# Kernel optimization log

Hardware: AMD Instinct MI355X
Metric: run time of the kernel (lower is better)

The kernel has to match this reference:

```python
import jax, jax.numpy as jnp
import numpy as np

EPS = 1e-8


def setup_inputs() -> dict:
    key = jax.random.key(0)
    ks = jax.random.split(key, 8)
    B, N, D = 8, 1024, 256
    x = jax.random.normal(ks[0], (B, N, D), dtype=jnp.float32)
    y = jax.random.normal(ks[1], (B, N, D), dtype=jnp.float32)
    coords = jax.random.normal(ks[2], (N, N, 6), dtype=jnp.float32)
    # xavier-ish init for U, kaiming-ish for S1/S2
    U = jax.random.normal(ks[3], (D, D), dtype=jnp.float32) * (1.0 / np.sqrt(D))
    S1 = jax.random.normal(ks[4], (D, 1), dtype=jnp.float32)
    S2 = jax.random.normal(ks[5], (D, 1), dtype=jnp.float32)
    gating = jnp.asarray(1.0, dtype=jnp.float32)
    h_temp = jnp.asarray(0.1, dtype=jnp.float32)
    p_temp = jnp.asarray(1.0, dtype=jnp.float32)
    # trunc_normal_(a=0, b=1): std-normal truncated to [0, 1]
    pos_emb = jax.random.truncated_normal(ks[6], 0.0, 1.0, (N, 6, 1)).astype(jnp.float32)
    return {"x": x, "y": y, "coords": coords, "U": U, "S1": S1, "S2": S2,
            "gating": gating, "h_temp": h_temp, "p_temp": p_temp, "pos_emb": pos_emb}


def _spectral(x, U, S):
    # x @ U.T @ diag(|S|) @ U  ==  ((x @ U.T) * |S|) @ U
    s = jnp.abs(S[:, 0])
    return ((x @ U.T) * s) @ U


def reference(x, y, coords, U, S1, S2, gating, h_temp, p_temp, pos_emb):
    B, N, D = x.shape
    scale = D ** (-0.5)
    xs = jnp.stack([_spectral(x, U, S1), _spectral(x, U, S2)], axis=1)  # [B,2,N,D]
    # patch attention scores: [B,2,N,N]
    patch_score = jax.nn.softmax(jnp.einsum('bknd,bmd->bknm', xs, y) * scale, axis=-1)
    # positional scores, shared across batch and the 2 spectral branches: [N,N]
    pos_logits = -jnp.abs(p_temp) * jnp.einsum('nmc,ncq->nm', coords, pos_emb)
    pos_score = jax.nn.softmax(pos_logits, axis=-1)
    g = jax.nn.sigmoid(gating)
    attn = (1.0 - g) * patch_score + g * pos_score[None, None]  # [B,2,N,N]
    # entropy over key axis -> [B,N,2]
    entropy = jnp.sum(-attn * jnp.log(attn + EPS), axis=-1).transpose(0, 2, 1)
    hmap = 2.0 - 2.0 * jax.nn.sigmoid(h_temp * entropy)  # [B,N,2]
    fgbg = hmap[..., 0] >= hmap[..., 1]
    route = jax.lax.stop_gradient(
        jnp.stack([fgbg, ~fgbg], axis=-1).astype(hmap.dtype))  # [B,N,2]
    heat_map = jnp.sum(hmap * route, axis=-1, keepdims=True)  # [B,N,1]
    attn_sel = jnp.sum(attn * route.transpose(0, 2, 1)[..., None], axis=1)  # [B,N,N]
    out = attn_sel @ y  # [B,N,D]
    return (out, heat_map)
```

## Files before the change

### kernel.cpp

```cpp
#include <hip/hip_runtime.h>
#include <hip/hip_bf16.h>


#define NB 8
#define NN_ 1024
#define ND 256

typedef __bf16 bf16x8 __attribute__((ext_vector_type(8)));
typedef __bf16 bf16x4 __attribute__((ext_vector_type(4)));
typedef float f32x4 __attribute__((ext_vector_type(4)));

__device__ inline float wred_sum(float v) {
#pragma unroll
    for (int o = 32; o; o >>= 1) v += __shfl_xor(v, o, 64);
    return v;
}
__device__ inline float wred_max(float v) {
#pragma unroll
    for (int o = 32; o; o >>= 1) v = fmaxf(v, __shfl_xor(v, o, 64));
    return v;
}
__device__ inline float bred_sum(float v, float* red) {
    v = wred_sum(v);
    int w = threadIdx.x >> 6;
    __syncthreads();
    if ((threadIdx.x & 63) == 0) red[w] = v;
    __syncthreads();
    return red[0] + red[1] + red[2] + red[3];
}
__device__ inline float bred_max(float v, float* red) {
    v = wred_max(v);
    int w = threadIdx.x >> 6;
    __syncthreads();
    if ((threadIdx.x & 63) == 0) red[w] = v;
    __syncthreads();
    return fmaxf(fmaxf(red[0], red[1]), fmaxf(red[2], red[3]));
}

__global__ __launch_bounds__(256) void pos_kernel(
    const float* __restrict__ coords, const float* __restrict__ pos_emb,
    const float* __restrict__ p_temp, float* __restrict__ posS) {
    __shared__ float red[4];
    const int n = blockIdx.x;
    const int tid = threadIdx.x;
    const float pt = -fabsf(p_temp[0]);
    float pe[6];
#pragma unroll
    for (int c = 0; c < 6; ++c) pe[c] = pos_emb[n * 6 + c];
    const float* cr = coords + (long)n * NN_ * 6;
    float l[4];
#pragma unroll
    for (int j = 0; j < 4; ++j) {
        const int m = tid * 4 + j;
        const float* cp = cr + m * 6;
        float d = 0.f;
#pragma unroll
        for (int c = 0; c < 6; ++c) d += cp[c] * pe[c];
        l[j] = pt * d;
    }
    float mx = fmaxf(fmaxf(l[0], l[1]), fmaxf(l[2], l[3]));
    mx = bred_max(mx, red);
    float e[4], s = 0.f;
#pragma unroll
    for (int j = 0; j < 4; ++j) { e[j] = expf(l[j] - mx); s += e[j]; }
    s = bred_sum(s, red);
    const float inv = 1.f / s;
    float4 o;
    o.x = e[0] * inv; o.y = e[1] * inv; o.z = e[2] * inv; o.w = e[3] * inv;
    *(float4*)(posS + (long)n * NN_ + tid * 4) = o;
}

__global__ __launch_bounds__(256) void conv_split(
    const float* __restrict__ src, __bf16* __restrict__ hi,
    __bf16* __restrict__ lo, int n4) {
    int i = blockIdx.x * 256 + threadIdx.x;
    const int stride = gridDim.x * 256;
    for (; i < n4; i += stride) {
        float4 v = ((const float4*)src)[i];
        bf16x4 h, l;
        h[0] = (__bf16)v.x; l[0] = (__bf16)(v.x - (float)h[0]);
        h[1] = (__bf16)v.y; l[1] = (__bf16)(v.y - (float)h[1]);
        h[2] = (__bf16)v.z; l[2] = (__bf16)(v.z - (float)h[2]);
        h[3] = (__bf16)v.w; l[3] = (__bf16)(v.w - (float)h[3]);
        ((bf16x4*)hi)[i] = h;
        ((bf16x4*)lo)[i] = l;
    }
}

__global__ __launch_bounds__(256) void conv_U(
    const float* __restrict__ U, const float* __restrict__ S1,
    const float* __restrict__ S2, __bf16* __restrict__ Uh, __bf16* __restrict__ Ul,
    __bf16* __restrict__ Wh, __bf16* __restrict__ Wl) {
    const int n = blockIdx.x, k = threadIdx.x;
    float u = U[n * ND + k];
    __bf16 h = (__bf16)u;
    Uh[n * ND + k] = h; Ul[n * ND + k] = (__bf16)(u - (float)h);
    float ukn = U[k * ND + n];
    float w1 = ukn * fabsf(S1[k]);
    float w2 = ukn * fabsf(S2[k]);
    __bf16 h1 = (__bf16)w1, h2 = (__bf16)w2;
    Wh[n * ND + k] = h1;             Wl[n * ND + k] = (__bf16)(w1 - (float)h1);
    Wh[65536 + n * ND + k] = h2;     Wl[65536 + n * ND + k] = (__bf16)(w2 - (float)h2);
}

__global__ __launch_bounds__(256) void prep_y(
    const float* __restrict__ y, __bf16* __restrict__ yt,
    __bf16* __restrict__ Yh, __bf16* __restrict__ Yl) {
    __shared__ __bf16 t[64][72];
    const int b = blockIdx.z;
    const int m0 = blockIdx.x * 64, d0 = blockIdx.y * 64;
    const int tid = threadIdx.x;
    const int c = tid & 15;
    const int r = tid >> 4;
#pragma unroll
    for (int p = 0; p < 4; ++p) {
        const int row = r + p * 16;
        const long gi = ((long)b * NN_ + m0 + row) * ND + d0 + c * 4;
        float4 v = *(const float4*)(y + gi);
        bf16x4 h, l;
        h[0] = (__bf16)v.x; l[0] = (__bf16)(v.x - (float)h[0]);
        h[1] = (__bf16)v.y; l[1] = (__bf16)(v.y - (float)h[1]);
        h[2] = (__bf16)v.z; l[2] = (__bf16)(v.z - (float)h[2]);
        h[3] = (__bf16)v.w; l[3] = (__bf16)(v.w - (float)h[3]);
        *(bf16x4*)(Yh + gi) = h;
        *(bf16x4*)(Yl + gi) = l;
        t[c * 4 + 0][row] = h[0]; t[c * 4 + 1][row] = h[1];
        t[c * 4 + 2][row] = h[2]; t[c * 4 + 3][row] = h[3];
    }
    __syncthreads();
#pragma unroll
    for (int p = 0; p < 4; ++p) {
        const int d = r + p * 16;
        bf16x4 o;
        o[0] = t[d][c * 4 + 0]; o[1] = t[d][c * 4 + 1];
        o[2] = t[d][c * 4 + 2]; o[3] = t[d][c * 4 + 3];
        *(bf16x4*)(yt + ((long)b * ND + d0 + d) * NN_ + m0 + c * 4) = o;
    }
}

template <int BN, bool SPLIT, int OUTM>
__global__ __launch_bounds__(256) void mgemm(
    const __bf16* __restrict__ Ah, const __bf16* __restrict__ Al,
    const __bf16* __restrict__ Bh, const __bf16* __restrict__ Bl,
    float* __restrict__ C, __bf16* __restrict__ Ch, __bf16* __restrict__ Cl,
    int M, int N, int K,
    long sA1, long sA2, int divA, long sB1, int divB, long sC, float alpha) {
    constexpr int BM = 128, BK = 32, RS = 40;
    constexpr int NBUF = SPLIT ? 2 : 1;
    constexpr int NF = BN / 32;
    __shared__ __bf16 As[NBUF][BM * RS];
    __shared__ __bf16 Bs[NBUF][BN * RS];

    const int z = blockIdx.z;
    const long aoff = (long)(z / divA) * sA1 + (long)(z % divA) * sA2;
    const long boff = (long)(z / divB) * sB1;
    Ah += aoff; if (SPLIT) Al += aoff;
    Bh += boff; if (SPLIT) Bl += boff;

    const int tid = threadIdx.x;
    const int bm = blockIdx.y * BM, bn = blockIdx.x * BN;
    const int wave = tid >> 6, lane = tid & 63;
    const int wm = wave >> 1, wn = wave & 1;
    const int quad = lane >> 4, l16 = lane & 15;

    f32x4 acc[4][NF];
#pragma unroll
    for (int i = 0; i < 4; ++i)
#pragma unroll
        for (int j = 0; j < NF; ++j) acc[i][j] = (f32x4){0.f, 0.f, 0.f, 0.f};

    const int arow = tid >> 1, ak = (tid & 1) * 16;

    for (int k0 = 0; k0 < K; k0 += BK) {
        {
            const long g = (long)(bm + arow) * K + k0 + ak;
            *(bf16x8*)&As[0][arow * RS + ak] = *(const bf16x8*)(Ah + g);
            *(bf16x8*)&As[0][arow * RS + ak + 8] = *(const bf16x8*)(Ah + g + 8);
            if (SPLIT) {
                *(bf16x8*)&As[1][arow * RS + ak] = *(const bf16x8*)(Al + g);
                *(bf16x8*)&As[1][arow * RS + ak + 8] = *(const bf16x8*)(Al + g + 8);
            }
        }
        if (BN == 128) {
            const long g = (long)(bn + arow) * K + k0 + ak;
            *(bf16x8*)&Bs[0][arow * RS + ak] = *(const bf16x8*)(Bh + g);
            *(bf16x8*)&Bs[0][arow * RS + ak + 8] = *(const bf16x8*)(Bh + g + 8);
            if (SPLIT) {
                *(bf16x8*)&Bs[1][arow * RS + ak] = *(const bf16x8*)(Bl + g);
                *(bf16x8*)&Bs[1][arow * RS + ak + 8] = *(const bf16x8*)(Bl + g + 8);
            }
        } else {
            const int brow = tid >> 2, bk = (tid & 3) * 8;
            const long g = (long)(bn + brow) * K + k0 + bk;
            *(bf16x8*)&Bs[0][brow * RS + bk] = *(const bf16x8*)(Bh + g);
            if (SPLIT)
                *(bf16x8*)&Bs[1][brow * RS + bk] = *(const bf16x8*)(Bl + g);
        }
        __syncthreads();

        bf16x8 a_h[4], a_l[4], b_h[NF], b_l[NF];
#pragma unroll
        for (int mi = 0; mi < 4; ++mi) {
            const int r = (wm * 64 + mi * 16 + l16) * RS + quad * 8;
            a_h[mi] = *(const bf16x8*)&As[0][r];
            if (SPLIT) a_l[mi] = *(const bf16x8*)&As[1][r];
        }
#pragma unroll
        for (int ni = 0; ni < NF; ++ni) {
            const int r = (wn * (BN / 2) + ni * 16 + l16) * RS + quad * 8;
            b_h[ni] = *(const bf16x8*)&Bs[0][r];
            if (SPLIT) b_l[ni] = *(const bf16x8*)&Bs[1][r];
        }
#pragma unroll
        for (int mi = 0; mi < 4; ++mi)
#pragma unroll
            for (int ni = 0; ni < NF; ++ni) {
                acc[mi][ni] = __builtin_amdgcn_mfma_f32_16x16x32_bf16(
                    a_h[mi], b_h[ni], acc[mi][ni], 0, 0, 0);
                if (SPLIT) {
                    acc[mi][ni] = __builtin_amdgcn_mfma_f32_16x16x32_bf16(
                        a_h[mi], b_l[ni], acc[mi][ni], 0, 0, 0);
                    acc[mi][ni] = __builtin_amdgcn_mfma_f32_16x16x32_bf16(
                        a_l[mi], b_h[ni], acc[mi][ni], 0, 0, 0);
                }
            }
        __syncthreads();
    }

    C += (long)z * sC; Ch += (long)z * sC; Cl += (long)z * sC;
#pragma unroll
    for (int mi = 0; mi < 4; ++mi) {
        const int row0 = bm + wm * 64 + mi * 16 + quad * 4;
#pragma unroll
        for (int ni = 0; ni < NF; ++ni) {
            const int col = bn + wn * (BN / 2) + ni * 16 + l16;
#pragma unroll
            for (int r = 0; r < 4; ++r) {
                const float v = acc[mi][ni][r] * alpha;
                const long idx = (long)(row0 + r) * N + col;
                if (OUTM == 0) {
                    C[idx] = v;
                } else {
                    const __bf16 h = (__bf16)v;
                    Ch[idx] = h;
                    Cl[idx] = (__bf16)(v - (float)h);
                }
            }
        }
    }
}

__global__ __launch_bounds__(256) void blend_kernel(
    const float* __restrict__ S, const float* __restrict__ pos,
    const float* __restrict__ gating, const float* __restrict__ h_temp,
    float* __restrict__ heat, __bf16* __restrict__ Pb) {
    __shared__ float red[4];
    const int bn = blockIdx.x;
    const int b = bn >> 10, n = bn & 1023;
    const float* S0 = S + ((long)(b * 2 + 0) * NN_ + n) * NN_;
    const float* S1 = S + ((long)(b * 2 + 1) * NN_ + n) * NN_;
    const int tid = threadIdx.x;

    float4 l0 = *(const float4*)(S0 + tid * 4);
    float4 l1 = *(const float4*)(S1 + tid * 4);
    float4 pv = *(const float4*)(pos + (long)n * NN_ + tid * 4);

    float m0 = fmaxf(fmaxf(l0.x, l0.y), fmaxf(l0.z, l0.w));
    m0 = bred_max(m0, red);
    float e0x = expf(l0.x - m0), e0y = expf(l0.y - m0),
          e0z = expf(l0.z - m0), e0w = expf(l0.w - m0);
    float s0 = bred_sum(e0x + e0y + e0z + e0w, red);
    const float i0 = 1.f / s0;
    float m1 = fmaxf(fmaxf(l1.x, l1.y), fmaxf(l1.z, l1.w));
    m1 = bred_max(m1, red);
    float e1x = expf(l1.x - m1), e1y = expf(l1.y - m1),
          e1z = expf(l1.z - m1), e1w = expf(l1.w - m1);
    float s1 = bred_sum(e1x + e1y + e1z + e1w, red);
    const float i1 = 1.f / s1;

    const float g = 1.f / (1.f + expf(-gating[0]));
    const float cg = 1.f - g;

    float a0[4], a1[4];
    a0[0] = cg * (e0x * i0) + g * pv.x; a0[1] = cg * (e0y * i0) + g * pv.y;
    a0[2] = cg * (e0z * i0) + g * pv.z; a0[3] = cg * (e0w * i0) + g * pv.w;
    a1[0] = cg * (e1x * i1) + g * pv.x; a1[1] = cg * (e1y * i1) + g * pv.y;
    a1[2] = cg * (e1z * i1) + g * pv.z; a1[3] = cg * (e1w * i1) + g * pv.w;

    float ent0 = 0.f, ent1 = 0.f;
#pragma unroll
    for (int j = 0; j < 4; ++j) {
        ent0 -= a0[j] * logf(a0[j] + 1e-8f);
        ent1 -= a1[j] * logf(a1[j] + 1e-8f);
    }
    ent0 = bred_sum(ent0, red);
    ent1 = bred_sum(ent1, red);

    const float ht = h_temp[0];
    const float hm0 = 2.f - 2.f / (1.f + expf(-ht * ent0));
    const float hm1 = 2.f - 2.f / (1.f + expf(-ht * ent1));
    const bool fg = (hm0 >= hm1);
    if (tid == 0) heat[bn] = fg ? hm0 : hm1;

    bf16x4 o;
    o[0] = (__bf16)(fg ? a0[0] : a1[0]);
    o[1] = (__bf16)(fg ? a0[1] : a1[1]);
    o[2] = (__bf16)(fg ? a0[2] : a1[2]);
    o[3] = (__bf16)(fg ? a0[3] : a1[3]);
    *(bf16x4*)(Pb + ((long)b * NN_ + n) * NN_ + tid * 4) = o;
}

extern "C" void kernel_launch(void* const* d_in, const int* in_sizes, int n_in,
                              void* d_out, int out_size, void* d_ws, size_t ws_size,
                              hipStream_t stream) {
    const float* x      = (const float*)d_in[0];
    const float* y      = (const float*)d_in[1];
    const float* coords = (const float*)d_in[2];
    const float* U      = (const float*)d_in[3];
    const float* S1p    = (const float*)d_in[4];
    const float* S2p    = (const float*)d_in[5];
    const float* gating = (const float*)d_in[6];
    const float* h_temp = (const float*)d_in[7];
    const float* p_temp = (const float*)d_in[8];
    const float* pos_emb= (const float*)d_in[9];

    float* out  = (float*)d_out;
    float* heat = out + (long)NB * NN_ * ND;

    char* ws = (char*)d_ws;
    const long MB = 1 << 20;
    float*  Sf  = (float*)(ws);
    float*  pos = (float*)(ws + 64 * MB);
    __bf16* Xh  = (__bf16*)(ws + 68 * MB);
    __bf16* Xl  = (__bf16*)(ws + 72 * MB);
    __bf16* XSh = (__bf16*)(ws + 68 * MB);
    __bf16* XSl = (__bf16*)(ws + 76 * MB);
    __bf16* Pb  = (__bf16*)(ws + 68 * MB);
    __bf16* yt  = (__bf16*)(ws + 84 * MB);
    __bf16* Yh  = (__bf16*)(ws + 88 * MB);
    __bf16* Yl  = (__bf16*)(ws + 92 * MB);
    __bf16* Th  = (__bf16*)(ws + 96 * MB);
    __bf16* Tl  = (__bf16*)(ws + 100 * MB);
    __bf16* Uh  = (__bf16*)(ws + 104 * MB);
    __bf16* Ul  = Uh + 65536;
    __bf16* Wh  = Uh + 2 * 65536;
    __bf16* Wl  = Uh + 4 * 65536;

    const long ND2 = (long)NN_ * ND;
    const long BND = (long)NB * ND2;

    pos_kernel<<<dim3(NN_), 256, 0, stream>>>(coords, pos_emb, p_temp, pos);
    conv_split<<<dim3(2048), 256, 0, stream>>>(x, Xh, Xl, (int)(BND / 4));
    prep_y<<<dim3(16, 4, NB), 256, 0, stream>>>(y, yt, Yh, Yl);
    conv_U<<<dim3(ND), ND, 0, stream>>>(U, S1p, S2p, Uh, Ul, Wh, Wl);

    mgemm<64, true, 1><<<dim3(4, 64, 1), 256, 0, stream>>>(
        Xh, Xl, Uh, Ul, nullptr, Th, Tl, NB * NN_, ND, ND,
        0, 0, 1, 0, 1, 0, 1.0f);

    mgemm<64, true, 1><<<dim3(4, 64, 2), 256, 0, stream>>>(
        Th, Tl, Wh, Wl, nullptr, XSh, XSl, NB * NN_, ND, ND,
        0, 0, 1, 65536, 1, BND, 1.0f);

    mgemm<128, true, 0><<<dim3(8, 8, NB * 2), 256, 0, stream>>>(
        XSh, XSl, Yh, Yl, Sf, nullptr, nullptr, NN_, NN_, ND,
        ND2, BND, 2, ND2, 2, (long)NN_ * NN_, 0.0625f);

    blend_kernel<<<dim3(NB * NN_), 256, 0, stream>>>(Sf, pos, gating, h_temp, heat, Pb);

    mgemm<64, false, 0><<<dim3(4, 8, NB), 256, 0, stream>>>(
        Pb, nullptr, yt, nullptr, out, nullptr, nullptr, NN_, ND, NN_,
        (long)NN_ * NN_, 0, 1, ND2, 1, ND2, 1.0f);

    (void)in_sizes; (void)n_in; (void)out_size; (void)ws_size;
}
```

Before: 224.2 us.

## Fold spectral projections into precomputed matrices and load GEMM tiles via global_load_lds

Precomputes M_s = U^T diag(|S|) U once per call in a small kernel, so x@M replaces two chained GEMMs and the intermediate T buffers are dropped. The GEMM kernel now loads tiles straight into LDS with global_load_lds using an XOR-swizzled, unpadded layout, and moves the barrier to the top of the loop. The positional kernel switches to coalesced strided rows with float2 loads. The M build is a naive serial loop of 256 iterations per thread and adds some rounding from the different factorisation.

```diff
diff --git a/kernel.cpp b/kernel.cpp
--- a/kernel.cpp
+++ b/kernel.cpp
@@ -1,5 +1,6 @@
 #include <hip/hip_runtime.h>
 #include <hip/hip_bf16.h>
+#include <stdint.h>
 
 
 #define NB 8
@@ -9,6 +10,12 @@
 typedef __bf16 bf16x8 __attribute__((ext_vector_type(8)));
 typedef __bf16 bf16x4 __attribute__((ext_vector_type(4)));
 typedef float f32x4 __attribute__((ext_vector_type(4)));
+
+__device__ inline void gl_lds(const __bf16* g, __bf16* l) {
+    auto gp = (const __attribute__((address_space(1))) uint32_t*)(uintptr_t)g;
+    auto lp = (__attribute__((address_space(3))) uint32_t*)(uintptr_t)l;
+    __builtin_amdgcn_global_load_lds(gp, lp, 16, 0, 0);
+}
 
 __device__ inline float wred_sum(float v) {
 #pragma unroll
@@ -51,12 +58,11 @@
     float l[4];
 #pragma unroll
     for (int j = 0; j < 4; ++j) {
-        const int m = tid * 4 + j;
-        const float* cp = cr + m * 6;
-        float d = 0.f;
-#pragma unroll
-        for (int c = 0; c < 6; ++c) d += cp[c] * pe[c];
-        l[j] = pt * d;
+        const int m = j * 256 + tid;
+        const float2* cp = (const float2*)(cr + (long)m * 6);
+        float2 c0 = cp[0], c1 = cp[1], c2 = cp[2];
+        l[j] = pt * (c0.x * pe[0] + c0.y * pe[1] + c1.x * pe[2] +
+                     c1.y * pe[3] + c2.x * pe[4] + c2.y * pe[5]);
     }
     float mx = fmaxf(fmaxf(l[0], l[1]), fmaxf(l[2], l[3]));
     mx = bred_max(mx, red);
@@ -65,9 +71,8 @@
     for (int j = 0; j < 4; ++j) { e[j] = expf(l[j] - mx); s += e[j]; }
     s = bred_sum(s, red);
     const float inv = 1.f / s;
-    float4 o;
-    o.x = e[0] * inv; o.y = e[1] * inv; o.z = e[2] * inv; o.w = e[3] * inv;
-    *(float4*)(posS + (long)n * NN_ + tid * 4) = o;
+#pragma unroll
+    for (int j = 0; j < 4; ++j) posS[(long)n * NN_ + j * 256 + tid] = e[j] * inv;
 }
 
 __global__ __launch_bounds__(256) void conv_split(
@@ -87,20 +92,21 @@
     }
 }
 
-__global__ __launch_bounds__(256) void conv_U(
+__global__ __launch_bounds__(256) void build_M(
     const float* __restrict__ U, const float* __restrict__ S1,
-    const float* __restrict__ S2, __bf16* __restrict__ Uh, __bf16* __restrict__ Ul,
-    __bf16* __restrict__ Wh, __bf16* __restrict__ Wl) {
-    const int n = blockIdx.x, k = threadIdx.x;
-    float u = U[n * ND + k];
-    __bf16 h = (__bf16)u;
-    Uh[n * ND + k] = h; Ul[n * ND + k] = (__bf16)(u - (float)h);
-    float ukn = U[k * ND + n];
-    float w1 = ukn * fabsf(S1[k]);
-    float w2 = ukn * fabsf(S2[k]);
-    __bf16 h1 = (__bf16)w1, h2 = (__bf16)w2;
-    Wh[n * ND + k] = h1;             Wl[n * ND + k] = (__bf16)(w1 - (float)h1);
-    Wh[65536 + n * ND + k] = h2;     Wl[65536 + n * ND + k] = (__bf16)(w2 - (float)h2);
+    const float* __restrict__ S2, __bf16* __restrict__ Mh,
+    __bf16* __restrict__ Ml) {
+    const int n = blockIdx.x, j = threadIdx.x;
+    float a1 = 0.f, a2 = 0.f;
+    for (int c = 0; c < ND; ++c) {
+        const float un = U[c * ND + n];
+        const float uj = U[c * ND + j];
+        a1 = fmaf(fabsf(S1[c]) * un, uj, a1);
+        a2 = fmaf(fabsf(S2[c]) * un, uj, a2);
+    }
+    const __bf16 h1 = (__bf16)a1, h2 = (__bf16)a2;
+    Mh[n * ND + j] = h1;            Ml[n * ND + j] = (__bf16)(a1 - (float)h1);
+    Mh[65536 + n * ND + j] = h2;    Ml[65536 + n * ND + j] = (__bf16)(a2 - (float)h2);
 }
 
 __global__ __launch_bounds__(256) void prep_y(
@@ -145,11 +151,11 @@
     float* __restrict__ C, __bf16* __restrict__ Ch, __bf16* __restrict__ Cl,
     int M, int N, int K,
     long sA1, long sA2, int divA, long sB1, int divB, long sC, float alpha) {
-    constexpr int BM = 128, BK = 32, RS = 40;
+    constexpr int BM = 128, BK = 32;
     constexpr int NBUF = SPLIT ? 2 : 1;
     constexpr int NF = BN / 32;
-    __shared__ __bf16 As[NBUF][BM * RS];
-    __shared__ __bf16 Bs[NBUF][BN * RS];
+    __shared__ __bf16 As[NBUF * BM * BK];
+    __shared__ __bf16 Bs[NBUF * BN * BK];
 
     const int z = blockIdx.z;
     const long aoff = (long)(z / divA) * sA1 + (long)(z % divA) * sA2;
@@ -169,47 +175,54 @@
 #pragma unroll
         for (int j = 0; j < NF; ++j) acc[i][j] = (f32x4){0.f, 0.f, 0.f, 0.f};
 
-    const int arow = tid >> 1, ak = (tid & 1) * 16;
+    const int srow = lane >> 2;
+    const int slot = lane & 3;
 
     for (int k0 = 0; k0 < K; k0 += BK) {
-        {
-            const long g = (long)(bm + arow) * K + k0 + ak;
-            *(bf16x8*)&As[0][arow * RS + ak] = *(const bf16x8*)(Ah + g);
-            *(bf16x8*)&As[0][arow * RS + ak + 8] = *(const bf16x8*)(Ah + g + 8);
-            if (SPLIT) {
-                *(bf16x8*)&As[1][arow * RS + ak] = *(const bf16x8*)(Al + g);
-                *(bf16x8*)&As[1][arow * RS + ak + 8] = *(const bf16x8*)(Al + g + 8);
-            }
+        __syncthreads();
+#pragma unroll
+        for (int i = 0; i < 2; ++i) {
+            const int r0 = wave * 32 + i * 16;
+            const int row = r0 + srow;
+            const int chunk = slot ^ ((row >> 1) & 3);
+            const long g = (long)(bm + row) * K + k0 + chunk * 8;
+            gl_lds(Ah + g, &As[r0 * 32]);
+            if (SPLIT) gl_lds(Al + g, &As[BM * BK + r0 * 32]);
         }
         if (BN == 128) {
-            const long g = (long)(bn + arow) * K + k0 + ak;
-            *(bf16x8*)&Bs[0][arow * RS + ak] = *(const bf16x8*)(Bh + g);
-            *(bf16x8*)&Bs[0][arow * RS + ak + 8] = *(const bf16x8*)(Bh + g + 8);
-            if (SPLIT) {
-                *(bf16x8*)&Bs[1][arow * RS + ak] = *(const bf16x8*)(Bl + g);
-                *(bf16x8*)&Bs[1][arow * RS + ak + 8] = *(const bf16x8*)(Bl + g + 8);
+#pragma unroll
+            for (int i = 0; i < 2; ++i) {
+                const int r0 = wave * 32 + i * 16;
+                const int row = r0 + srow;
+                const int chunk = slot ^ ((row >> 1) & 3);
+                const long g = (long)(bn + row) * K + k0 + chunk * 8;
+                gl_lds(Bh + g, &Bs[r0 * 32]);
+                if (SPLIT) gl_lds(Bl + g, &Bs[BN * BK + r0 * 32]);
             }
         } else {
-            const int brow = tid >> 2, bk = (tid & 3) * 8;
-            const long g = (long)(bn + brow) * K + k0 + bk;
-            *(bf16x8*)&Bs[0][brow * RS + bk] = *(const bf16x8*)(Bh + g);
-            if (SPLIT)
-                *(bf16x8*)&Bs[1][brow * RS + bk] = *(const bf16x8*)(Bl + g);
+            const int r0 = wave * 16;
+            const int row = r0 + srow;
+            const int chunk = slot ^ ((row >> 1) & 3);
+            const long g = (long)(bn + row) * K + k0 + chunk * 8;
+            gl_lds(Bh + g, &Bs[r0 * 32]);
+            if (SPLIT) gl_lds(Bl + g, &Bs[BN * BK + r0 * 32]);
         }
         __syncthreads();
 
         bf16x8 a_h[4], a_l[4], b_h[NF], b_l[NF];
 #pragma unroll
         for (int mi = 0; mi < 4; ++mi) {
-            const int r = (wm * 64 + mi * 16 + l16) * RS + quad * 8;
-            a_h[mi] = *(const bf16x8*)&As[0][r];
-            if (SPLIT) a_l[mi] = *(const bf16x8*)&As[1][r];
+            const int row = wm * 64 + mi * 16 + l16;
+            const int off = row * 32 + ((quad ^ ((row >> 1) & 3)) * 8);
+            a_h[mi] = *(const bf16x8*)&As[off];
+            if (SPLIT) a_l[mi] = *(const bf16x8*)&As[BM * BK + off];
         }
 #pragma unroll
         for (int ni = 0; ni < NF; ++ni) {
-            const int r = (wn * (BN / 2) + ni * 16 + l16) * RS + quad * 8;
-            b_h[ni] = *(const bf16x8*)&Bs[0][r];
-            if (SPLIT) b_l[ni] = *(const bf16x8*)&Bs[1][r];
+            const int row = wn * (BN / 2) + ni * 16 + l16;
+            const int off = row * 32 + ((quad ^ ((row >> 1) & 3)) * 8);
+            b_h[ni] = *(const bf16x8*)&Bs[off];
+            if (SPLIT) b_l[ni] = *(const bf16x8*)&Bs[BN * BK + off];
         }
 #pragma unroll
         for (int mi = 0; mi < 4; ++mi)
@@ -224,7 +237,6 @@
                         a_l[mi], b_h[ni], acc[mi][ni], 0, 0, 0);
                 }
             }
-        __syncthreads();
     }
 
     C += (long)z * sC; Ch += (long)z * sC; Cl += (long)z * sC;
@@ -333,18 +345,14 @@
     float*  pos = (float*)(ws + 64 * MB);
     __bf16* Xh  = (__bf16*)(ws + 68 * MB);
     __bf16* Xl  = (__bf16*)(ws + 72 * MB);
-    __bf16* XSh = (__bf16*)(ws + 68 * MB);
-    __bf16* XSl = (__bf16*)(ws + 76 * MB);
+    __bf16* XSh = (__bf16*)(ws + 76 * MB);
+    __bf16* XSl = (__bf16*)(ws + 84 * MB);
     __bf16* Pb  = (__bf16*)(ws + 68 * MB);
-    __bf16* yt  = (__bf16*)(ws + 84 * MB);
-    __bf16* Yh  = (__bf16*)(ws + 88 * MB);
-    __bf16* Yl  = (__bf16*)(ws + 92 * MB);
-    __bf16* Th  = (__bf16*)(ws + 96 * MB);
-    __bf16* Tl  = (__bf16*)(ws + 100 * MB);
-    __bf16* Uh  = (__bf16*)(ws + 104 * MB);
-    __bf16* Ul  = Uh + 65536;
-    __bf16* Wh  = Uh + 2 * 65536;
-    __bf16* Wl  = Uh + 4 * 65536;
+    __bf16* yt  = (__bf16*)(ws + 92 * MB);
+    __bf16* Yh  = (__bf16*)(ws + 96 * MB);
+    __bf16* Yl  = (__bf16*)(ws + 100 * MB);
+    __bf16* Mh  = (__bf16*)(ws + 104 * MB);
+    __bf16* Ml  = Mh + 2 * 65536;
 
     const long ND2 = (long)NN_ * ND;
     const long BND = (long)NB * ND2;
@@ -352,14 +360,10 @@
     pos_kernel<<<dim3(NN_), 256, 0, stream>>>(coords, pos_emb, p_temp, pos);
     conv_split<<<dim3(2048), 256, 0, stream>>>(x, Xh, Xl, (int)(BND / 4));
     prep_y<<<dim3(16, 4, NB), 256, 0, stream>>>(y, yt, Yh, Yl);
-    conv_U<<<dim3(ND), ND, 0, stream>>>(U, S1p, S2p, Uh, Ul, Wh, Wl);
-
-    mgemm<64, true, 1><<<dim3(4, 64, 1), 256, 0, stream>>>(
-        Xh, Xl, Uh, Ul, nullptr, Th, Tl, NB * NN_, ND, ND,
-        0, 0, 1, 0, 1, 0, 1.0f);
+    build_M<<<dim3(ND), ND, 0, stream>>>(U, S1p, S2p, Mh, Ml);
 
     mgemm<64, true, 1><<<dim3(4, 64, 2), 256, 0, stream>>>(
-        Th, Tl, Wh, Wl, nullptr, XSh, XSl, NB * NN_, ND, ND,
+        Xh, Xl, Mh, Ml, nullptr, XSh, XSl, NB * NN_, ND, ND,
         0, 0, 1, 65536, 1, BND, 1.0f);
 
     mgemm<128, true, 0><<<dim3(8, 8, NB * 2), 256, 0, stream>>>(
```

Result: no change. 220.5 us (-1.7%).
